# Optimization experiments

Measured on AMD Instinct MI355X. Metric: run time of the kernel, lower is better.

The kernel has to match this reference:

```python
import jax, jax.numpy as jnp
import numpy as np

D = 1024
H = 16
HD = D // H


def setup_inputs() -> dict:
    key = jax.random.key(0)
    ks = jax.random.split(key, 11)
    B, S = 4, 1024
    s = 0.02
    return {
        "q": jax.random.normal(ks[0], (B, S, D), jnp.float32),
        "k": jax.random.normal(ks[1], (B, S, D), jnp.float32),
        "v": jax.random.normal(ks[2], (B, S, D), jnp.float32),
        "Wq": jax.random.normal(ks[3], (D, D), jnp.float32) * s,
        "bq": jnp.zeros((D,), jnp.float32),
        "Wk": jax.random.normal(ks[4], (D, D), jnp.float32) * s,
        "bk": jnp.zeros((D,), jnp.float32),
        "Wv": jax.random.normal(ks[5], (D, D), jnp.float32) * s,
        "bv": jnp.zeros((D,), jnp.float32),
        "Wo": jax.random.normal(ks[6], (D, D), jnp.float32) * s,
        "bo": jnp.zeros((D,), jnp.float32),
    }


def _split_heads(x):
    # [B, S, D] -> [B, H, S, HD]
    B, S, _ = x.shape
    return x.reshape(B, S, H, HD).transpose(0, 2, 1, 3)


def reference(q, k, v, Wq, bq, Wk, bk, Wv, bv, Wo, bo):
    # Projections followed by ReLU (faithful to the original module)
    qh = _split_heads(jax.nn.relu(q @ Wq + bq))
    kh = _split_heads(jax.nn.relu(k @ Wk + bk))
    vh = _split_heads(jax.nn.relu(v @ Wv + bv))
    # NOTE: original scales by sqrt(input_dim), not sqrt(head_dim)
    scale = 1.0 / jnp.sqrt(jnp.float32(D))
    scores = jnp.einsum("bhsd,bhtd->bhst", qh, kh) * scale  # [B,H,S,S]
    weights = jax.nn.softmax(scores, axis=-1)  # dropout is identity in eval
    attn = jnp.einsum("bhst,bhtd->bhsd", weights, vh)  # [B,H,S,HD]
    B, _, S, _ = attn.shape
    attn = attn.transpose(0, 2, 1, 3).reshape(B, S, D)
    return attn @ Wo + bo
```

## Files before the change

kernel.cpp:

```cpp
#include <hip/hip_runtime.h>
#include <math.h>

#define Dm 1024
#define Hn 16
#define HDn 64
#define Sn 1024

typedef __attribute__((ext_vector_type(8))) __bf16 bf16x8;
typedef __attribute__((ext_vector_type(4))) float floatx4;

__device__ __forceinline__ void async_ld16(void* lds, const void* g) {
    __builtin_amdgcn_global_load_lds(
        (const __attribute__((address_space(1))) void*)g,
        (__attribute__((address_space(3))) void*)lds,
        16, 0, 0);
}

__global__ __launch_bounds__(256) void cast_qkv_kernel(
    const float* __restrict__ a, const float* __restrict__ b, const float* __restrict__ c,
    __bf16* __restrict__ oa, __bf16* __restrict__ ob, __bf16* __restrict__ oc)
{
    const int lin = blockIdx.x * 256 + threadIdx.x;
    const float* src = (blockIdx.y == 0) ? a : (blockIdx.y == 1) ? b : c;
    __bf16* dst = (blockIdx.y == 0) ? oa : (blockIdx.y == 1) ? ob : oc;
    const float4 v0 = ((const float4*)src)[lin * 2];
    const float4 v1 = ((const float4*)src)[lin * 2 + 1];
    bf16x8 o;
    o[0] = (__bf16)v0.x; o[1] = (__bf16)v0.y; o[2] = (__bf16)v0.z; o[3] = (__bf16)v0.w;
    o[4] = (__bf16)v1.x; o[5] = (__bf16)v1.y; o[6] = (__bf16)v1.z; o[7] = (__bf16)v1.w;
    ((bf16x8*)dst)[lin] = o;
}

__global__ __launch_bounds__(256) void cast_wt_kernel(
    const float* __restrict__ W0, const float* __restrict__ W1,
    const float* __restrict__ W2, const float* __restrict__ W3,
    __bf16* __restrict__ O0, __bf16* __restrict__ O1,
    __bf16* __restrict__ O2, __bf16* __restrict__ O3)
{
    __shared__ float sT[64][65];
    const int z = blockIdx.z;
    const float* W = (z == 0) ? W0 : (z == 1) ? W1 : (z == 2) ? W2 : W3;
    __bf16* O = (z == 0) ? O0 : (z == 1) ? O1 : (z == 2) ? O2 : O3;

    const int tid = threadIdx.x;
    const int bi = blockIdx.y * 64, bj = blockIdx.x * 64;
    const int colr = tid & 63, rowg = tid >> 6;

    #pragma unroll
    for (int i = 0; i < 16; ++i) {
        const int kk = i * 4 + rowg;
        sT[kk][colr] = W[(size_t)(bi + kk) * Dm + bj + colr];
    }
    __syncthreads();
    #pragma unroll
    for (int i = 0; i < 16; ++i) {
        const int rn = i * 4 + rowg;
        O[(size_t)(bj + rn) * Dm + bi + colr] = (__bf16)sT[colr][rn];
    }
}

struct GemmArgs {
    const __bf16* X[3];
    const __bf16* WT[3];
    const float*  bias[3];
    void*         out[3];
    int   layout[3];
    int   relu[3];
    float esc[3];
};

__global__ __launch_bounds__(256) void gemm_bf16_kernel(GemmArgs args)
{
    __shared__ __align__(16) __bf16 sA[128 * 32];
    __shared__ __align__(16) __bf16 sB[128 * 32];

    const int z = blockIdx.z;
    const __bf16* __restrict__ Xb  = args.X[z];
    const __bf16* __restrict__ WTb = args.WT[z];
    const float*  __restrict__ bias = args.bias[z];
    void* __restrict__ outp = args.out[z];
    const int layout = args.layout[z];
    const int do_relu = args.relu[z];
    const float escale = args.esc[z];

    const int tid = threadIdx.x;
    const int bm = blockIdx.y * 128, bn = blockIdx.x * 128;
    const int lane = tid & 63;
    const int wave = tid >> 6;
    const int wm = (wave & 1) * 64;
    const int wn = (wave >> 1) * 64;
    const int l15 = lane & 15, quad = lane >> 4;

    floatx4 acc[4][4];
    #pragma unroll
    for (int mi = 0; mi < 4; ++mi)
        #pragma unroll
        for (int ni = 0; ni < 4; ++ni)
            acc[mi][ni] = (floatx4){0.f, 0.f, 0.f, 0.f};

    const int c0 = tid,       r0 = c0 >> 2, q0 = (c0 & 3) ^ (r0 & 3);
    const int c1 = tid + 256, r1 = c1 >> 2, q1 = (c1 & 3) ^ (r1 & 3);
    const __bf16* gA0 = Xb  + (size_t)(bm + r0) * Dm + q0 * 8;
    const __bf16* gA1 = Xb  + (size_t)(bm + r1) * Dm + q1 * 8;
    const __bf16* gB0 = WTb + (size_t)(bn + r0) * Dm + q0 * 8;
    const __bf16* gB1 = WTb + (size_t)(bn + r1) * Dm + q1 * 8;
    char* lA0 = (char*)sA + (tid & 192) * 16;
    char* lA1 = (char*)sA + (256 + (tid & 192)) * 16;
    char* lB0 = (char*)sB + (tid & 192) * 16;
    char* lB1 = (char*)sB + (256 + (tid & 192)) * 16;

    const __bf16* fA[4];
    const __bf16* fB[4];
    #pragma unroll
    for (int mi = 0; mi < 4; ++mi) {
        const int r = wm + mi * 16 + l15;
        fA[mi] = sA + r * 32 + ((quad ^ (r & 3)) * 8);
    }
    #pragma unroll
    for (int ni = 0; ni < 4; ++ni) {
        const int r = wn + ni * 16 + l15;
        fB[ni] = sB + r * 32 + ((quad ^ (r & 3)) * 8);
    }

    for (int kt = 0; kt < Dm; kt += 32) {
        async_ld16(lA0, gA0 + kt);
        async_ld16(lA1, gA1 + kt);
        async_ld16(lB0, gB0 + kt);
        async_ld16(lB1, gB1 + kt);
        __syncthreads();

        bf16x8 af[4], bfr[4];
        #pragma unroll
        for (int mi = 0; mi < 4; ++mi) af[mi] = *(const bf16x8*)fA[mi];
        #pragma unroll
        for (int ni = 0; ni < 4; ++ni) bfr[ni] = *(const bf16x8*)fB[ni];
        #pragma unroll
        for (int mi = 0; mi < 4; ++mi)
            #pragma unroll
            for (int ni = 0; ni < 4; ++ni)
                acc[mi][ni] = __builtin_amdgcn_mfma_f32_16x16x32_bf16(
                    af[mi], bfr[ni], acc[mi][ni], 0, 0, 0);
        __syncthreads();
    }

    #pragma unroll
    for (int mi = 0; mi < 4; ++mi) {
        #pragma unroll
        for (int ni = 0; ni < 4; ++ni) {
            const int n = bn + wn + ni * 16 + l15;
            const float bv = bias[n];
            const int h = n >> 6, d = n & 63;
            #pragma unroll
            for (int reg = 0; reg < 4; ++reg) {
                const int m = bm + wm + mi * 16 + quad * 4 + reg;
                const int b = m >> 10, s = m & 1023;
                float v = acc[mi][ni][reg] + bv;
                if (do_relu) v = fmaxf(v, 0.0f);
                v *= escale;
                if (layout == 0)
                    ((__bf16*)outp)[((size_t)(b * Hn + h) * 1024 + s) * 64 + d] = (__bf16)v;
                else if (layout == 1)
                    ((__bf16*)outp)[((size_t)(b * Hn + h) * 64 + d) * 1024 + s] = (__bf16)v;
                else
                    ((float*)outp)[(size_t)m * 1024 + n] = v;
            }
        }
    }
}

__global__ __launch_bounds__(256, 2) void flash_attn_kernel(
    const __bf16* __restrict__ Qh,
    const __bf16* __restrict__ Kh,
    const __bf16* __restrict__ Vt,
    __bf16* __restrict__ ctx)
{
    __shared__ __align__(16) char sKV[2][16384];
    __shared__ __align__(16) __bf16 sP[4][32 * 64];

    const int tid = threadIdx.x;
    const int wave = tid >> 6, lane = tid & 63;
    const int l15 = lane & 15, quad = lane >> 4;
    const int b = blockIdx.z, h = blockIdx.y;
    const int bh = b * Hn + h;
    const int qb = blockIdx.x * 128 + wave * 32;

    bf16x8 aQ[2][2];
    #pragma unroll
    for (int mi = 0; mi < 2; ++mi)
        #pragma unroll
        for (int ks = 0; ks < 2; ++ks)
            aQ[mi][ks] = *(const bf16x8*)(Qh +
                (size_t)(bh * Sn + qb + mi * 16 + l15) * 64 + ks * 32 + quad * 8);

    const int s0 = tid, s1 = tid + 256;
    const int r0 = s0 >> 3, q0c = (s0 & 7) ^ (r0 & 7);
    const int r1 = s1 >> 3, q1c = (s1 & 7) ^ (r1 & 7);
    const __bf16* gK0 = Kh + (size_t)(bh * Sn + r0) * 64 + q0c * 8;
    const __bf16* gK1 = Kh + (size_t)(bh * Sn + r1) * 64 + q1c * 8;
    const __bf16* gV0 = Vt + (size_t)(bh * 64 + r0) * Sn + q0c * 8;
    const __bf16* gV1 = Vt + (size_t)(bh * 64 + r1) * Sn + q1c * 8;
    const int wofs = (tid & 192) * 16;

    floatx4 oacc[2][4];
    #pragma unroll
    for (int mi = 0; mi < 2; ++mi)
        #pragma unroll
        for (int nf = 0; nf < 4; ++nf)
            oacc[mi][nf] = (floatx4){0.f, 0.f, 0.f, 0.f};
    float lsum[2][4];
    #pragma unroll
    for (int mi = 0; mi < 2; ++mi)
        #pragma unroll
        for (int r = 0; r < 4; ++r) lsum[mi][r] = 0.0f;

    __bf16* sPw = sP[wave];

    {
        char* bK = sKV[0];
        char* bV = sKV[0] + 8192;
        async_ld16(bK + wofs,        gK0);
        async_ld16(bK + 4096 + wofs, gK1);
        async_ld16(bV + wofs,        gV0);
        async_ld16(bV + 4096 + wofs, gV1);
    }

    int cur = 0;
    for (int it = 0; it < 16; ++it) {
        __syncthreads();

        if (it + 1 < 16) {
            const int t0n = (it + 1) * 64;
            char* bK = sKV[cur ^ 1];
            char* bV = sKV[cur ^ 1] + 8192;
            async_ld16(bK + wofs,        gK0 + (size_t)t0n * 64);
            async_ld16(bK + 4096 + wofs, gK1 + (size_t)t0n * 64);
            async_ld16(bV + wofs,        gV0 + t0n);
            async_ld16(bV + 4096 + wofs, gV1 + t0n);
        }

        const __bf16* sK = (const __bf16*)sKV[cur];
        const __bf16* sV = (const __bf16*)(sKV[cur] + 8192);

        floatx4 sc[2][4];
        #pragma unroll
        for (int mi = 0; mi < 2; ++mi)
            #pragma unroll
            for (int nf = 0; nf < 4; ++nf)
                sc[mi][nf] = (floatx4){0.f, 0.f, 0.f, 0.f};
        #pragma unroll
        for (int ks = 0; ks < 2; ++ks) {
            bf16x8 bK[4];
            #pragma unroll
            for (int nf = 0; nf < 4; ++nf) {
                const int n = nf * 16 + l15;
                bK[nf] = *(const bf16x8*)(sK + (n * 8 + (((ks << 2) + quad) ^ (n & 7))) * 8);
            }
            #pragma unroll
            for (int mi = 0; mi < 2; ++mi)
                #pragma unroll
                for (int nf = 0; nf < 4; ++nf)
                    sc[mi][nf] = __builtin_amdgcn_mfma_f32_16x16x32_bf16(
                        aQ[mi][ks], bK[nf], sc[mi][nf], 0, 0, 0);
        }

        #pragma unroll
        for (int mi = 0; mi < 2; ++mi)
            #pragma unroll
            for (int nf = 0; nf < 4; ++nf) {
                const int t = nf * 16 + l15;
                #pragma unroll
                for (int r = 0; r < 4; ++r) {
                    const float p = __builtin_amdgcn_exp2f(fminf(sc[mi][nf][r], 126.0f));
                    const __bf16 pb = (__bf16)p;
                    lsum[mi][r] += (float)pb;
                    const int rr = mi * 16 + quad * 4 + r;
                    sPw[(rr * 8 + ((t >> 3) ^ (rr & 7))) * 8 + (t & 7)] = pb;
                }
            }

        #pragma unroll
        for (int ks = 0; ks < 2; ++ks) {
            bf16x8 aP[2], bV[4];
            #pragma unroll
            for (int mi = 0; mi < 2; ++mi) {
                const int r = mi * 16 + l15;
                aP[mi] = *(const bf16x8*)(sPw + (r * 8 + (((ks << 2) + quad) ^ (r & 7))) * 8);
            }
            #pragma unroll
            for (int nf = 0; nf < 4; ++nf) {
                const int n = nf * 16 + l15;
                bV[nf] = *(const bf16x8*)(sV + (n * 8 + (((ks << 2) + quad) ^ (n & 7))) * 8);
            }
            #pragma unroll
            for (int mi = 0; mi < 2; ++mi)
                #pragma unroll
                for (int nf = 0; nf < 4; ++nf)
                    oacc[mi][nf] = __builtin_amdgcn_mfma_f32_16x16x32_bf16(
                        aP[mi], bV[nf], oacc[mi][nf], 0, 0, 0);
        }

        cur ^= 1;
    }

    float linv[2][4];
    #pragma unroll
    for (int mi = 0; mi < 2; ++mi)
        #pragma unroll
        for (int r = 0; r < 4; ++r) {
            float l = lsum[mi][r];
            l += __shfl_xor(l, 1, 64);
            l += __shfl_xor(l, 2, 64);
            l += __shfl_xor(l, 4, 64);
            l += __shfl_xor(l, 8, 64);
            linv[mi][r] = 1.0f / l;
        }

    #pragma unroll
    for (int mi = 0; mi < 2; ++mi)
        #pragma unroll
        for (int nf = 0; nf < 4; ++nf) {
            const int d = h * 64 + nf * 16 + l15;
            #pragma unroll
            for (int reg = 0; reg < 4; ++reg) {
                const int s = qb + mi * 16 + quad * 4 + reg;
                ctx[(size_t)(b * Sn + s) * Dm + d] =
                    (__bf16)(oacc[mi][nf][reg] * linv[mi][reg]);
            }
        }
}

extern "C" void kernel_launch(void* const* d_in, const int* in_sizes, int n_in,
                              void* d_out, int out_size, void* d_ws, size_t ws_size,
                              hipStream_t stream)
{
    const float* q  = (const float*)d_in[0];
    const float* k  = (const float*)d_in[1];
    const float* v  = (const float*)d_in[2];
    const float* Wq = (const float*)d_in[3];
    const float* bq = (const float*)d_in[4];
    const float* Wk = (const float*)d_in[5];
    const float* bk = (const float*)d_in[6];
    const float* Wv = (const float*)d_in[7];
    const float* bv = (const float*)d_in[8];
    const float* Wo = (const float*)d_in[9];
    const float* bo = (const float*)d_in[10];

    char* ws = (char*)d_ws;
    const size_t MB = 1024 * 1024;
    __bf16* qb_ = (__bf16*)(ws);
    __bf16* kb_ = (__bf16*)(ws + 8 * MB);
    __bf16* vb_ = (__bf16*)(ws + 16 * MB);
    __bf16* WTq = (__bf16*)(ws + 24 * MB);
    __bf16* WTk = (__bf16*)(ws + 26 * MB);
    __bf16* WTv = (__bf16*)(ws + 28 * MB);
    __bf16* WTo = (__bf16*)(ws + 30 * MB);
    __bf16* Qh  = (__bf16*)(ws + 32 * MB);
    __bf16* Kh  = (__bf16*)(ws + 40 * MB);
    __bf16* Vt  = (__bf16*)(ws + 48 * MB);
    __bf16* ctx = (__bf16*)(ws + 56 * MB);

    cast_qkv_kernel<<<dim3(2048, 3), 256, 0, stream>>>(q, k, v, qb_, kb_, vb_);
    cast_wt_kernel<<<dim3(16, 16, 4), 256, 0, stream>>>(Wq, Wk, Wv, Wo,
                                                        WTq, WTk, WTv, WTo);

    const float QSCALE = 0.0450842200f;

    GemmArgs qkv;
    qkv.X[0] = qb_;  qkv.X[1] = kb_;  qkv.X[2] = vb_;
    qkv.WT[0] = WTq; qkv.WT[1] = WTk; qkv.WT[2] = WTv;
    qkv.bias[0] = bq; qkv.bias[1] = bk; qkv.bias[2] = bv;
    qkv.out[0] = Qh;  qkv.out[1] = Kh;  qkv.out[2] = Vt;
    qkv.layout[0] = 0; qkv.layout[1] = 0; qkv.layout[2] = 1;
    qkv.relu[0] = 1;   qkv.relu[1] = 1;   qkv.relu[2] = 1;
    qkv.esc[0] = QSCALE; qkv.esc[1] = 1.0f; qkv.esc[2] = 1.0f;
    gemm_bf16_kernel<<<dim3(8, 32, 3), 256, 0, stream>>>(qkv);

    flash_attn_kernel<<<dim3(8, Hn, 4), 256, 0, stream>>>(Qh, Kh, Vt, ctx);

    GemmArgs og;
    og.X[0] = ctx;  og.X[1] = ctx;  og.X[2] = ctx;
    og.WT[0] = WTo; og.WT[1] = WTo; og.WT[2] = WTo;
    og.bias[0] = bo; og.bias[1] = bo; og.bias[2] = bo;
    og.out[0] = d_out; og.out[1] = d_out; og.out[2] = d_out;
    og.layout[0] = 3; og.layout[1] = 3; og.layout[2] = 3;
    og.relu[0] = 0;   og.relu[1] = 0;   og.relu[2] = 0;
    og.esc[0] = 1.0f; og.esc[1] = 1.0f; og.esc[2] = 1.0f;
    gemm_bf16_kernel<<<dim3(8, 32, 1), 256, 0, stream>>>(og);
}
```

Measured before the change: 229.7 us.

## Merge prep kernels, swizzle block order, split-K output GEMM with atomics

```diff
diff --git a/kernel.cpp b/kernel.cpp
--- a/kernel.cpp
+++ b/kernel.cpp
@@ -16,46 +16,52 @@
         16, 0, 0);
 }
 
-__global__ __launch_bounds__(256) void cast_qkv_kernel(
-    const float* __restrict__ a, const float* __restrict__ b, const float* __restrict__ c,
-    __bf16* __restrict__ oa, __bf16* __restrict__ ob, __bf16* __restrict__ oc)
-{
-    const int lin = blockIdx.x * 256 + threadIdx.x;
-    const float* src = (blockIdx.y == 0) ? a : (blockIdx.y == 1) ? b : c;
-    __bf16* dst = (blockIdx.y == 0) ? oa : (blockIdx.y == 1) ? ob : oc;
-    const float4 v0 = ((const float4*)src)[lin * 2];
-    const float4 v1 = ((const float4*)src)[lin * 2 + 1];
-    bf16x8 o;
-    o[0] = (__bf16)v0.x; o[1] = (__bf16)v0.y; o[2] = (__bf16)v0.z; o[3] = (__bf16)v0.w;
-    o[4] = (__bf16)v1.x; o[5] = (__bf16)v1.y; o[6] = (__bf16)v1.z; o[7] = (__bf16)v1.w;
-    ((bf16x8*)dst)[lin] = o;
-}
-
-__global__ __launch_bounds__(256) void cast_wt_kernel(
-    const float* __restrict__ W0, const float* __restrict__ W1,
-    const float* __restrict__ W2, const float* __restrict__ W3,
-    __bf16* __restrict__ O0, __bf16* __restrict__ O1,
-    __bf16* __restrict__ O2, __bf16* __restrict__ O3)
+struct PrepArgs {
+    const float* qkv[3];
+    __bf16*      qkv_o[3];
+    const float* W[4];
+    __bf16*      WT[4];
+    float*       out_zero;
+};
+
+__global__ __launch_bounds__(256) void prep_kernel(PrepArgs a)
 {
     __shared__ float sT[64][65];
-    const int z = blockIdx.z;
-    const float* W = (z == 0) ? W0 : (z == 1) ? W1 : (z == 2) ? W2 : W3;
-    __bf16* O = (z == 0) ? O0 : (z == 1) ? O1 : (z == 2) ? O2 : O3;
-
-    const int tid = threadIdx.x;
-    const int bi = blockIdx.y * 64, bj = blockIdx.x * 64;
-    const int colr = tid & 63, rowg = tid >> 6;
-
-    #pragma unroll
-    for (int i = 0; i < 16; ++i) {
-        const int kk = i * 4 + rowg;
-        sT[kk][colr] = W[(size_t)(bi + kk) * Dm + bj + colr];
-    }
-    __syncthreads();
-    #pragma unroll
-    for (int i = 0; i < 16; ++i) {
-        const int rn = i * 4 + rowg;
-        O[(size_t)(bj + rn) * Dm + bi + colr] = (__bf16)sT[colr][rn];
+    const int z = blockIdx.z, x = blockIdx.x, tid = threadIdx.x;
+
+    if (z < 3) {
+        const float* src = a.qkv[z];
+        __bf16* dst = a.qkv_o[z];
+        const int lin = x * 256 + tid;
+        const float4 v0 = ((const float4*)src)[lin * 2];
+        const float4 v1 = ((const float4*)src)[lin * 2 + 1];
+        bf16x8 o;
+        o[0] = (__bf16)v0.x; o[1] = (__bf16)v0.y; o[2] = (__bf16)v0.z; o[3] = (__bf16)v0.w;
+        o[4] = (__bf16)v1.x; o[5] = (__bf16)v1.y; o[6] = (__bf16)v1.z; o[7] = (__bf16)v1.w;
+        ((bf16x8*)dst)[lin] = o;
+    } else if (z < 7) {
+        if (x >= 256) return;
+        const float* W = a.W[z - 3];
+        __bf16* O = a.WT[z - 3];
+        const int bi = (x >> 4) * 64, bj = (x & 15) * 64;
+        const int colr = tid & 63, rowg = tid >> 6;
+        #pragma unroll
+        for (int i = 0; i < 16; ++i) {
+            const int kk = i * 4 + rowg;
+            sT[kk][colr] = W[(size_t)(bi + kk) * Dm + bj + colr];
+        }
+        __syncthreads();
+        #pragma unroll
+        for (int i = 0; i < 16; ++i) {
+            const int rn = i * 4 + rowg;
+            O[(size_t)(bj + rn) * Dm + bi + colr] = (__bf16)sT[colr][rn];
+        }
+    } else {
+        float4* o = (float4*)a.out_zero;
+        const int i = (x * 256 + tid) * 2;
+        const float4 zz = make_float4(0.f, 0.f, 0.f, 0.f);
+        o[i] = zz;
+        o[i + 1] = zz;
     }
 }
 
@@ -65,7 +71,6 @@
     const float*  bias[3];
     void*         out[3];
     int   layout[3];
-    int   relu[3];
     float esc[3];
 };
 
@@ -80,11 +85,13 @@
     const float*  __restrict__ bias = args.bias[z];
     void* __restrict__ outp = args.out[z];
     const int layout = args.layout[z];
-    const int do_relu = args.relu[z];
     const float escale = args.esc[z];
 
     const int tid = threadIdx.x;
-    const int bm = blockIdx.y * 128, bn = blockIdx.x * 128;
+    const int id = blockIdx.x + (blockIdx.y << 3);
+    const int bm = (((id & 7) << 2) | (id >> 6)) * 128;
+    const int bn = ((id >> 3) & 7) * 128;
+
     const int lane = tid & 63;
     const int wave = tid >> 6;
     const int wm = (wave & 1) * 64;
@@ -154,15 +161,98 @@
             for (int reg = 0; reg < 4; ++reg) {
                 const int m = bm + wm + mi * 16 + quad * 4 + reg;
                 const int b = m >> 10, s = m & 1023;
-                float v = acc[mi][ni][reg] + bv;
-                if (do_relu) v = fmaxf(v, 0.0f);
-                v *= escale;
+                float v = fmaxf(acc[mi][ni][reg] + bv, 0.0f) * escale;
                 if (layout == 0)
                     ((__bf16*)outp)[((size_t)(b * Hn + h) * 1024 + s) * 64 + d] = (__bf16)v;
-                else if (layout == 1)
+                else
                     ((__bf16*)outp)[((size_t)(b * Hn + h) * 64 + d) * 1024 + s] = (__bf16)v;
-                else
-                    ((float*)outp)[(size_t)m * 1024 + n] = v;
+            }
+        }
+    }
+}
+
+__global__ __launch_bounds__(256) void gemm_splitk_kernel(
+    const __bf16* __restrict__ Xb, const __bf16* __restrict__ WTb,
+    const float* __restrict__ bias, float* __restrict__ outp)
+{
+    __shared__ __align__(16) __bf16 sA[128 * 32];
+    __shared__ __align__(16) __bf16 sB[128 * 32];
+
+    const int tid = threadIdx.x;
+    const int kz = blockIdx.z;
+    const int id = blockIdx.x + (blockIdx.y << 3);
+    const int bm = (((id & 7) << 2) | (id >> 6)) * 128;
+    const int bn = ((id >> 3) & 7) * 128;
+
+    const int lane = tid & 63;
+    const int wave = tid >> 6;
+    const int wm = (wave & 1) * 64;
+    const int wn = (wave >> 1) * 64;
+    const int l15 = lane & 15, quad = lane >> 4;
+
+    floatx4 acc[4][4];
+    #pragma unroll
+    for (int mi = 0; mi < 4; ++mi)
+        #pragma unroll
+        for (int ni = 0; ni < 4; ++ni)
+            acc[mi][ni] = (floatx4){0.f, 0.f, 0.f, 0.f};
+
+    const int c0 = tid,       r0 = c0 >> 2, q0 = (c0 & 3) ^ (r0 & 3);
+    const int c1 = tid + 256, r1 = c1 >> 2, q1 = (c1 & 3) ^ (r1 & 3);
+    const int kofs = kz * 512;
+    const __bf16* gA0 = Xb  + (size_t)(bm + r0) * Dm + kofs + q0 * 8;
+    const __bf16* gA1 = Xb  + (size_t)(bm + r1) * Dm + kofs + q1 * 8;
+    const __bf16* gB0 = WTb + (size_t)(bn + r0) * Dm + kofs + q0 * 8;
+    const __bf16* gB1 = WTb + (size_t)(bn + r1) * Dm + kofs + q1 * 8;
+    char* lA0 = (char*)sA + (tid & 192) * 16;
+    char* lA1 = (char*)sA + (256 + (tid & 192)) * 16;
+    char* lB0 = (char*)sB + (tid & 192) * 16;
+    char* lB1 = (char*)sB + (256 + (tid & 192)) * 16;
+
+    const __bf16* fA[4];
+    const __bf16* fB[4];
+    #pragma unroll
+    for (int mi = 0; mi < 4; ++mi) {
+        const int r = wm + mi * 16 + l15;
+        fA[mi] = sA + r * 32 + ((quad ^ (r & 3)) * 8);
+    }
+    #pragma unroll
+    for (int ni = 0; ni < 4; ++ni) {
+        const int r = wn + ni * 16 + l15;
+        fB[ni] = sB + r * 32 + ((quad ^ (r & 3)) * 8);
+    }
+
+    for (int kt = 0; kt < 512; kt += 32) {
+        async_ld16(lA0, gA0 + kt);
+        async_ld16(lA1, gA1 + kt);
+        async_ld16(lB0, gB0 + kt);
+        async_ld16(lB1, gB1 + kt);
+        __syncthreads();
+
+        bf16x8 af[4], bfr[4];
+        #pragma unroll
+        for (int mi = 0; mi < 4; ++mi) af[mi] = *(const bf16x8*)fA[mi];
+        #pragma unroll
+        for (int ni = 0; ni < 4; ++ni) bfr[ni] = *(const bf16x8*)fB[ni];
+        #pragma unroll
+        for (int mi = 0; mi < 4; ++mi)
+            #pragma unroll
+            for (int ni = 0; ni < 4; ++ni)
+                acc[mi][ni] = __builtin_amdgcn_mfma_f32_16x16x32_bf16(
+                    af[mi], bfr[ni], acc[mi][ni], 0, 0, 0);
+        __syncthreads();
+    }
+
+    #pragma unroll
+    for (int mi = 0; mi < 4; ++mi) {
+        #pragma unroll
+        for (int ni = 0; ni < 4; ++ni) {
+            const int n = bn + wn + ni * 16 + l15;
+            const float bv = (kz == 0) ? bias[n] : 0.0f;
+            #pragma unroll
+            for (int reg = 0; reg < 4; ++reg) {
+                const int m = bm + wm + mi * 16 + quad * 4 + reg;
+                atomicAdd(outp + (size_t)m * 1024 + n, acc[mi][ni][reg] + bv);
             }
         }
     }
@@ -180,9 +270,12 @@
     const int tid = threadIdx.x;
     const int wave = tid >> 6, lane = tid & 63;
     const int l15 = lane & 15, quad = lane >> 4;
-    const int b = blockIdx.z, h = blockIdx.y;
-    const int bh = b * Hn + h;
-    const int qb = blockIdx.x * 128 + wave * 32;
+
+    const int id = blockIdx.x + (blockIdx.y << 3) + (blockIdx.z << 7);
+    const int kk = id >> 3;
+    const int bh = ((id & 7) << 3) | (kk & 7);
+    const int b = bh >> 4, h = bh & 15;
+    const int qb = (kk >> 3) * 128 + wave * 32;
 
     bf16x8 aQ[2][2];
     #pragma unroll
@@ -359,9 +452,13 @@
     __bf16* Vt  = (__bf16*)(ws + 48 * MB);
     __bf16* ctx = (__bf16*)(ws + 56 * MB);
 
-    cast_qkv_kernel<<<dim3(2048, 3), 256, 0, stream>>>(q, k, v, qb_, kb_, vb_);
-    cast_wt_kernel<<<dim3(16, 16, 4), 256, 0, stream>>>(Wq, Wk, Wv, Wo,
-                                                        WTq, WTk, WTv, WTo);
+    PrepArgs pa;
+    pa.qkv[0] = q; pa.qkv[1] = k; pa.qkv[2] = v;
+    pa.qkv_o[0] = qb_; pa.qkv_o[1] = kb_; pa.qkv_o[2] = vb_;
+    pa.W[0] = Wq; pa.W[1] = Wk; pa.W[2] = Wv; pa.W[3] = Wo;
+    pa.WT[0] = WTq; pa.WT[1] = WTk; pa.WT[2] = WTv; pa.WT[3] = WTo;
+    pa.out_zero = (float*)d_out;
+    prep_kernel<<<dim3(2048, 1, 8), 256, 0, stream>>>(pa);
 
     const float QSCALE = 0.0450842200f;
 
@@ -371,19 +468,11 @@
     qkv.bias[0] = bq; qkv.bias[1] = bk; qkv.bias[2] = bv;
     qkv.out[0] = Qh;  qkv.out[1] = Kh;  qkv.out[2] = Vt;
     qkv.layout[0] = 0; qkv.layout[1] = 0; qkv.layout[2] = 1;
-    qkv.relu[0] = 1;   qkv.relu[1] = 1;   qkv.relu[2] = 1;
     qkv.esc[0] = QSCALE; qkv.esc[1] = 1.0f; qkv.esc[2] = 1.0f;
     gemm_bf16_kernel<<<dim3(8, 32, 3), 256, 0, stream>>>(qkv);
 
-    flash_attn_kernel<<<dim3(8, Hn, 4), 256, 0, stream>>>(Qh, Kh, Vt, ctx);
-
-    GemmArgs og;
-    og.X[0] = ctx;  og.X[1] = ctx;  og.X[2] = ctx;
-    og.WT[0] = WTo; og.WT[1] = WTo; og.WT[2] = WTo;
-    og.bias[0] = bo; og.bias[1] = bo; og.bias[2] = bo;
-    og.out[0] = d_out; og.out[1] = d_out; og.out[2] = d_out;
-    og.layout[0] = 3; og.layout[1] = 3; og.layout[2] = 3;
-    og.relu[0] = 0;   og.relu[1] = 0;   og.relu[2] = 0;
-    og.esc[0] = 1.0f; og.esc[1] = 1.0f; og.esc[2] = 1.0f;
-    gemm_bf16_kernel<<<dim3(8, 32, 1), 256, 0, stream>>>(og);
-}
+    flash_attn_kernel<<<dim3(8, 16, 4), 256, 0, stream>>>(Qh, Kh, Vt, ctx);
+
+    gemm_splitk_kernel<<<dim3(8, 32, 2), 256, 0, stream>>>(
+        ctx, WTo, bo, (float*)d_out);
+}
```

New measurement: 228.1 us. No clear change (-0.7%).

## Merge prep kernels, shrink GEMM N-tile to 64, and remap block order

Applied to the files above, without the earlier changes.

```diff
diff --git a/kernel.cpp b/kernel.cpp
--- a/kernel.cpp
+++ b/kernel.cpp
@@ -16,46 +16,45 @@
         16, 0, 0);
 }
 
-__global__ __launch_bounds__(256) void cast_qkv_kernel(
-    const float* __restrict__ a, const float* __restrict__ b, const float* __restrict__ c,
-    __bf16* __restrict__ oa, __bf16* __restrict__ ob, __bf16* __restrict__ oc)
-{
-    const int lin = blockIdx.x * 256 + threadIdx.x;
-    const float* src = (blockIdx.y == 0) ? a : (blockIdx.y == 1) ? b : c;
-    __bf16* dst = (blockIdx.y == 0) ? oa : (blockIdx.y == 1) ? ob : oc;
-    const float4 v0 = ((const float4*)src)[lin * 2];
-    const float4 v1 = ((const float4*)src)[lin * 2 + 1];
-    bf16x8 o;
-    o[0] = (__bf16)v0.x; o[1] = (__bf16)v0.y; o[2] = (__bf16)v0.z; o[3] = (__bf16)v0.w;
-    o[4] = (__bf16)v1.x; o[5] = (__bf16)v1.y; o[6] = (__bf16)v1.z; o[7] = (__bf16)v1.w;
-    ((bf16x8*)dst)[lin] = o;
-}
-
-__global__ __launch_bounds__(256) void cast_wt_kernel(
-    const float* __restrict__ W0, const float* __restrict__ W1,
-    const float* __restrict__ W2, const float* __restrict__ W3,
-    __bf16* __restrict__ O0, __bf16* __restrict__ O1,
-    __bf16* __restrict__ O2, __bf16* __restrict__ O3)
+struct PrepArgs {
+    const float* qkv[3];
+    __bf16*      qkv_o[3];
+    const float* W[4];
+    __bf16*      WT[4];
+};
+
+__global__ __launch_bounds__(256) void prep_kernel(PrepArgs a)
 {
     __shared__ float sT[64][65];
-    const int z = blockIdx.z;
-    const float* W = (z == 0) ? W0 : (z == 1) ? W1 : (z == 2) ? W2 : W3;
-    __bf16* O = (z == 0) ? O0 : (z == 1) ? O1 : (z == 2) ? O2 : O3;
-
-    const int tid = threadIdx.x;
-    const int bi = blockIdx.y * 64, bj = blockIdx.x * 64;
-    const int colr = tid & 63, rowg = tid >> 6;
-
-    #pragma unroll
-    for (int i = 0; i < 16; ++i) {
-        const int kk = i * 4 + rowg;
-        sT[kk][colr] = W[(size_t)(bi + kk) * Dm + bj + colr];
-    }
-    __syncthreads();
-    #pragma unroll
-    for (int i = 0; i < 16; ++i) {
-        const int rn = i * 4 + rowg;
-        O[(size_t)(bj + rn) * Dm + bi + colr] = (__bf16)sT[colr][rn];
+    const int z = blockIdx.z, x = blockIdx.x, tid = threadIdx.x;
+
+    if (z < 3) {
+        const float* src = a.qkv[z];
+        __bf16* dst = a.qkv_o[z];
+        const int lin = x * 256 + tid;
+        const float4 v0 = ((const float4*)src)[lin * 2];
+        const float4 v1 = ((const float4*)src)[lin * 2 + 1];
+        bf16x8 o;
+        o[0] = (__bf16)v0.x; o[1] = (__bf16)v0.y; o[2] = (__bf16)v0.z; o[3] = (__bf16)v0.w;
+        o[4] = (__bf16)v1.x; o[5] = (__bf16)v1.y; o[6] = (__bf16)v1.z; o[7] = (__bf16)v1.w;
+        ((bf16x8*)dst)[lin] = o;
+    } else {
+        if (x >= 256) return;
+        const float* W = a.W[z - 3];
+        __bf16* O = a.WT[z - 3];
+        const int bi = (x >> 4) * 64, bj = (x & 15) * 64;
+        const int colr = tid & 63, rowg = tid >> 6;
+        #pragma unroll
+        for (int i = 0; i < 16; ++i) {
+            const int kk = i * 4 + rowg;
+            sT[kk][colr] = W[(size_t)(bi + kk) * Dm + bj + colr];
+        }
+        __syncthreads();
+        #pragma unroll
+        for (int i = 0; i < 16; ++i) {
+            const int rn = i * 4 + rowg;
+            O[(size_t)(bj + rn) * Dm + bi + colr] = (__bf16)sT[colr][rn];
+        }
     }
 }
 
@@ -65,14 +64,13 @@
     const float*  bias[3];
     void*         out[3];
     int   layout[3];
-    int   relu[3];
     float esc[3];
 };
 
 __global__ __launch_bounds__(256) void gemm_bf16_kernel(GemmArgs args)
 {
     __shared__ __align__(16) __bf16 sA[128 * 32];
-    __shared__ __align__(16) __bf16 sB[128 * 32];
+    __shared__ __align__(16) __bf16 sB[64 * 32];
 
     const int z = blockIdx.z;
     const __bf16* __restrict__ Xb  = args.X[z];
@@ -80,44 +78,45 @@
     const float*  __restrict__ bias = args.bias[z];
     void* __restrict__ outp = args.out[z];
     const int layout = args.layout[z];
-    const int do_relu = args.relu[z];
     const float escale = args.esc[z];
 
     const int tid = threadIdx.x;
-    const int bm = blockIdx.y * 128, bn = blockIdx.x * 128;
+    const int id = blockIdx.x + (blockIdx.y << 4);
+    const int bm = (((id & 7) << 2) | (id >> 7)) * 128;
+    const int bn = ((id >> 3) & 15) * 64;
+
     const int lane = tid & 63;
     const int wave = tid >> 6;
     const int wm = (wave & 1) * 64;
-    const int wn = (wave >> 1) * 64;
+    const int wn = (wave >> 1) * 32;
     const int l15 = lane & 15, quad = lane >> 4;
 
-    floatx4 acc[4][4];
+    floatx4 acc[4][2];
     #pragma unroll
     for (int mi = 0; mi < 4; ++mi)
         #pragma unroll
-        for (int ni = 0; ni < 4; ++ni)
+        for (int ni = 0; ni < 2; ++ni)
             acc[mi][ni] = (floatx4){0.f, 0.f, 0.f, 0.f};
 
     const int c0 = tid,       r0 = c0 >> 2, q0 = (c0 & 3) ^ (r0 & 3);
     const int c1 = tid + 256, r1 = c1 >> 2, q1 = (c1 & 3) ^ (r1 & 3);
+    const int rB = tid >> 2,  qB = (tid & 3) ^ (rB & 3);
     const __bf16* gA0 = Xb  + (size_t)(bm + r0) * Dm + q0 * 8;
     const __bf16* gA1 = Xb  + (size_t)(bm + r1) * Dm + q1 * 8;
-    const __bf16* gB0 = WTb + (size_t)(bn + r0) * Dm + q0 * 8;
-    const __bf16* gB1 = WTb + (size_t)(bn + r1) * Dm + q1 * 8;
+    const __bf16* gB  = WTb + (size_t)(bn + rB) * Dm + qB * 8;
     char* lA0 = (char*)sA + (tid & 192) * 16;
     char* lA1 = (char*)sA + (256 + (tid & 192)) * 16;
-    char* lB0 = (char*)sB + (tid & 192) * 16;
-    char* lB1 = (char*)sB + (256 + (tid & 192)) * 16;
+    char* lB  = (char*)sB + (tid & 192) * 16;
 
     const __bf16* fA[4];
-    const __bf16* fB[4];
+    const __bf16* fB[2];
     #pragma unroll
     for (int mi = 0; mi < 4; ++mi) {
         const int r = wm + mi * 16 + l15;
         fA[mi] = sA + r * 32 + ((quad ^ (r & 3)) * 8);
     }
     #pragma unroll
-    for (int ni = 0; ni < 4; ++ni) {
+    for (int ni = 0; ni < 2; ++ni) {
         const int r = wn + ni * 16 + l15;
         fB[ni] = sB + r * 32 + ((quad ^ (r & 3)) * 8);
     }
@@ -125,19 +124,18 @@
     for (int kt = 0; kt < Dm; kt += 32) {
         async_ld16(lA0, gA0 + kt);
         async_ld16(lA1, gA1 + kt);
-        async_ld16(lB0, gB0 + kt);
-        async_ld16(lB1, gB1 + kt);
+        async_ld16(lB,  gB  + kt);
         __syncthreads();
 
-        bf16x8 af[4], bfr[4];
+        bf16x8 af[4], bfr[2];
         #pragma unroll
         for (int mi = 0; mi < 4; ++mi) af[mi] = *(const bf16x8*)fA[mi];
         #pragma unroll
-        for (int ni = 0; ni < 4; ++ni) bfr[ni] = *(const bf16x8*)fB[ni];
+        for (int ni = 0; ni < 2; ++ni) bfr[ni] = *(const bf16x8*)fB[ni];
         #pragma unroll
         for (int mi = 0; mi < 4; ++mi)
             #pragma unroll
-            for (int ni = 0; ni < 4; ++ni)
+            for (int ni = 0; ni < 2; ++ni)
                 acc[mi][ni] = __builtin_amdgcn_mfma_f32_16x16x32_bf16(
                     af[mi], bfr[ni], acc[mi][ni], 0, 0, 0);
         __syncthreads();
@@ -146,7 +144,7 @@
     #pragma unroll
     for (int mi = 0; mi < 4; ++mi) {
         #pragma unroll
-        for (int ni = 0; ni < 4; ++ni) {
+        for (int ni = 0; ni < 2; ++ni) {
             const int n = bn + wn + ni * 16 + l15;
             const float bv = bias[n];
             const int h = n >> 6, d = n & 63;
@@ -154,15 +152,15 @@
             for (int reg = 0; reg < 4; ++reg) {
                 const int m = bm + wm + mi * 16 + quad * 4 + reg;
                 const int b = m >> 10, s = m & 1023;
-                float v = acc[mi][ni][reg] + bv;
-                if (do_relu) v = fmaxf(v, 0.0f);
-                v *= escale;
-                if (layout == 0)
-                    ((__bf16*)outp)[((size_t)(b * Hn + h) * 1024 + s) * 64 + d] = (__bf16)v;
-                else if (layout == 1)
-                    ((__bf16*)outp)[((size_t)(b * Hn + h) * 64 + d) * 1024 + s] = (__bf16)v;
-                else
-                    ((float*)outp)[(size_t)m * 1024 + n] = v;
+                if (layout == 3) {
+                    ((float*)outp)[(size_t)m * 1024 + n] = acc[mi][ni][reg] + bv;
+                } else {
+                    float v = fmaxf(acc[mi][ni][reg] + bv, 0.0f) * escale;
+                    if (layout == 0)
+                        ((__bf16*)outp)[((size_t)(b * Hn + h) * 1024 + s) * 64 + d] = (__bf16)v;
+                    else
+                        ((__bf16*)outp)[((size_t)(b * Hn + h) * 64 + d) * 1024 + s] = (__bf16)v;
+                }
             }
         }
     }
@@ -180,9 +178,12 @@
     const int tid = threadIdx.x;
     const int wave = tid >> 6, lane = tid & 63;
     const int l15 = lane & 15, quad = lane >> 4;
-    const int b = blockIdx.z, h = blockIdx.y;
-    const int bh = b * Hn + h;
-    const int qb = blockIdx.x * 128 + wave * 32;
+
+    const int id = blockIdx.x + (blockIdx.y << 3) + (blockIdx.z << 7);
+    const int kk = id >> 3;
+    const int bh = ((id & 7) << 3) | (kk & 7);
+    const int b = bh >> 4, h = bh & 15;
+    const int qb = (kk >> 3) * 128 + wave * 32;
 
     bf16x8 aQ[2][2];
     #pragma unroll
@@ -359,9 +360,12 @@
     __bf16* Vt  = (__bf16*)(ws + 48 * MB);
     __bf16* ctx = (__bf16*)(ws + 56 * MB);
 
-    cast_qkv_kernel<<<dim3(2048, 3), 256, 0, stream>>>(q, k, v, qb_, kb_, vb_);
-    cast_wt_kernel<<<dim3(16, 16, 4), 256, 0, stream>>>(Wq, Wk, Wv, Wo,
-                                                        WTq, WTk, WTv, WTo);
+    PrepArgs pa;
+    pa.qkv[0] = q; pa.qkv[1] = k; pa.qkv[2] = v;
+    pa.qkv_o[0] = qb_; pa.qkv_o[1] = kb_; pa.qkv_o[2] = vb_;
+    pa.W[0] = Wq; pa.W[1] = Wk; pa.W[2] = Wv; pa.W[3] = Wo;
+    pa.WT[0] = WTq; pa.WT[1] = WTk; pa.WT[2] = WTv; pa.WT[3] = WTo;
+    prep_kernel<<<dim3(2048, 1, 7), 256, 0, stream>>>(pa);
 
     const float QSCALE = 0.0450842200f;
 
@@ -371,11 +375,10 @@
     qkv.bias[0] = bq; qkv.bias[1] = bk; qkv.bias[2] = bv;
     qkv.out[0] = Qh;  qkv.out[1] = Kh;  qkv.out[2] = Vt;
     qkv.layout[0] = 0; qkv.layout[1] = 0; qkv.layout[2] = 1;
-    qkv.relu[0] = 1;   qkv.relu[1] = 1;   qkv.relu[2] = 1;
     qkv.esc[0] = QSCALE; qkv.esc[1] = 1.0f; qkv.esc[2] = 1.0f;
-    gemm_bf16_kernel<<<dim3(8, 32, 3), 256, 0, stream>>>(qkv);
-
-    flash_attn_kernel<<<dim3(8, Hn, 4), 256, 0, stream>>>(Qh, Kh, Vt, ctx);
+    gemm_bf16_kernel<<<dim3(16, 32, 3), 256, 0, stream>>>(qkv);
+
+    flash_attn_kernel<<<dim3(8, 16, 4), 256, 0, stream>>>(Qh, Kh, Vt, ctx);
 
     GemmArgs og;
     og.X[0] = ctx;  og.X[1] = ctx;  og.X[2] = ctx;
@@ -383,7 +386,6 @@
     og.bias[0] = bo; og.bias[1] = bo; og.bias[2] = bo;
     og.out[0] = d_out; og.out[1] = d_out; og.out[2] = d_out;
     og.layout[0] = 3; og.layout[1] = 3; og.layout[2] = 3;
-    og.relu[0] = 0;   og.relu[1] = 0;   og.relu[2] = 0;
     og.esc[0] = 1.0f; og.esc[1] = 1.0f; og.esc[2] = 1.0f;
-    gemm_bf16_kernel<<<dim3(8, 32, 1), 256, 0, stream>>>(og);
-}
+    gemm_bf16_kernel<<<dim3(16, 32, 1), 256, 0, stream>>>(og);
+}
```

Result: no change. 231.2 us (+0.6%).
